# Kernel optimization log

Hardware: AMD Instinct MI355X
Metric: run time of the kernel (lower is better)

The kernel has to match this reference:

```python
import jax, jax.numpy as jnp
import numpy as np

EPS = 1e-5

def _act_quant(x):
    # per-token int8 absmax quantization with straight-through estimator
    scale = 127.0 / jnp.clip(jnp.max(jnp.abs(x), axis=-1, keepdims=True), EPS, None)
    q = jnp.clip(jnp.round(x * scale), -128.0, 127.0) / scale
    return x + jax.lax.stop_gradient(q - x)

def _weight_quant(w):
    # per-tensor ternary (1.58-bit) quantization with STE
    scale = 1.0 / jnp.clip(jnp.mean(jnp.abs(w)), EPS, None)
    q = jnp.clip(jnp.round(w * scale), -1.0, 1.0) / scale
    return w + jax.lax.stop_gradient(q - w)

def _bitlinear(x, w, b):
    y = jnp.einsum('bsd,od->bso', _act_quant(x), _weight_quant(w))
    return y + b

def setup_inputs() -> dict:
    key = jax.random.key(0)
    k1, k2, k3, k4, k5 = jax.random.split(key, 5)
    B, S, D, F = 8, 4096, 1024, 3072
    return {
        'x': jax.random.normal(k1, (B, S, D), dtype=jnp.float32),
        'up_w': jax.random.normal(k2, (F, D), dtype=jnp.float32) * 0.125,
        'up_b': jax.random.normal(k3, (F,), dtype=jnp.float32) * 0.01,
        'down_w': jax.random.normal(k4, (D, F), dtype=jnp.float32) * 0.125,
        'down_b': jax.random.normal(k5, (D,), dtype=jnp.float32) * 0.01,
    }

def reference(x, up_w, up_b, down_w, down_b):
    hidden = _bitlinear(x, up_w, up_b)          # [B,S,3072]
    hidden = jnp.square(jax.nn.relu(hidden))    # relu(h)^2
    return _bitlinear(hidden, down_w, down_b)   # [B,S,1024]
```

## Files before the change

kernel.cpp:

```cpp
#include <hip/hip_runtime.h>
#include <hip/hip_bf16.h>
#include <stdint.h>

#define EPS 1e-5f

typedef int v4i __attribute__((ext_vector_type(4)));
typedef int v16i __attribute__((ext_vector_type(16)));
typedef const __attribute__((address_space(1))) void g_void;
typedef __attribute__((address_space(3))) void l_void;

__device__ inline float block_max_nw(float v, int nw) {
    __shared__ float s[8];
#pragma unroll
    for (int o = 32; o; o >>= 1) v = fmaxf(v, __shfl_xor(v, o, 64));
    if ((threadIdx.x & 63) == 0) s[threadIdx.x >> 6] = v;
    __syncthreads();
    float m = s[0];
    for (int i = 1; i < nw; ++i) m = fmaxf(m, s[i]);
    return m;
}

__device__ inline float block_sum64x4(float v) {
    __shared__ float s[4];
#pragma unroll
    for (int o = 32; o; o >>= 1) v += __shfl_xor(v, o, 64);
    if ((threadIdx.x & 63) == 0) s[threadIdx.x >> 6] = v;
    __syncthreads();
    return s[0] + s[1] + s[2] + s[3];
}

__global__ __launch_bounds__(256) void abs_sum_part_k(const float4* __restrict__ w,
                                                      int n4, float* __restrict__ part) {
    float s = 0.0f;
    for (int i = blockIdx.x * 256 + threadIdx.x; i < n4; i += 1024 * 256) {
        float4 v = w[i];
        s += fabsf(v.x) + fabsf(v.y) + fabsf(v.z) + fabsf(v.w);
    }
    s = block_sum64x4(s);
    if (threadIdx.x == 0) part[blockIdx.x] = s;
}

__global__ __launch_bounds__(256) void abs_sum_final_k(const float* __restrict__ parts,
                                                       float* __restrict__ sums) {
    const float* p = parts + blockIdx.x * 1024;
    const int t = threadIdx.x;
    float s = p[t] + p[t + 256] + p[t + 512] + p[t + 768];
    s = block_sum64x4(s);
    if (t == 0) sums[blockIdx.x] = s;
}

__global__ __launch_bounds__(256) void wquant_k(const float4* __restrict__ w,
                                                char4* __restrict__ q,
                                                const float* __restrict__ sum) {
    const float mean = fmaxf(sum[0] * (1.0f / 3145728.0f), EPS);
    const float scale = 1.0f / mean;
    const int i = blockIdx.x * 256 + threadIdx.x;
    float4 v = w[i];
    char4 c;
    c.x = (signed char)(int)fmaxf(fminf(rintf(v.x * scale), 1.0f), -1.0f);
    c.y = (signed char)(int)fmaxf(fminf(rintf(v.y * scale), 1.0f), -1.0f);
    c.z = (signed char)(int)fmaxf(fminf(rintf(v.z * scale), 1.0f), -1.0f);
    c.w = (signed char)(int)fmaxf(fminf(rintf(v.w * scale), 1.0f), -1.0f);
    q[i] = c;
}

__global__ __launch_bounds__(256) void aquant_k(const float4* __restrict__ x,
                                                char4* __restrict__ q,
                                                float* __restrict__ deq) {
    const int row = blockIdx.x, t = threadIdx.x;
    const float4 v = x[(size_t)row * 256 + t];
    float m = fmaxf(fmaxf(fabsf(v.x), fabsf(v.y)), fmaxf(fabsf(v.z), fabsf(v.w)));
    m = block_max_nw(m, 4);
    const float mc = fmaxf(m, EPS);
    const float sc = 127.0f / mc;
    char4 c;
    c.x = (signed char)(int)fmaxf(fminf(rintf(v.x * sc), 127.0f), -128.0f);
    c.y = (signed char)(int)fmaxf(fminf(rintf(v.y * sc), 127.0f), -128.0f);
    c.z = (signed char)(int)fmaxf(fminf(rintf(v.z * sc), 127.0f), -128.0f);
    c.w = (signed char)(int)fmaxf(fminf(rintf(v.w * sc), 127.0f), -128.0f);
    q[(size_t)row * 256 + t] = c;
    if (t == 0) deq[row] = mc / 127.0f;
}

__global__ __launch_bounds__(384) void hquant_k(unsigned short* __restrict__ hid,
                                                float* __restrict__ deq) {
    const size_t row = blockIdx.x;
    const int t = threadIdx.x;
    unsigned short* rp = hid + row * 3072;
    const uint4 u = ((const uint4*)rp)[t];
    float v[8];
    {
        uint32_t uu[4] = {u.x, u.y, u.z, u.w};
#pragma unroll
        for (int i = 0; i < 4; ++i) {
            uint32_t lo = uu[i] << 16, hi = uu[i] & 0xFFFF0000u;
            v[2 * i]     = __uint_as_float(lo);
            v[2 * i + 1] = __uint_as_float(hi);
        }
    }
    float m = 0.0f;
#pragma unroll
    for (int i = 0; i < 8; ++i) m = fmaxf(m, fabsf(v[i]));
    m = block_max_nw(m, 6);
    const float mc = fmaxf(m, EPS);
    const float sc = 127.0f / mc;
    uint32_t p0 = 0, p1 = 0;
#pragma unroll
    for (int i = 0; i < 4; ++i) {
        int c = (int)fminf(rintf(v[i] * sc), 127.0f);
        p0 |= (uint32_t)(c & 255) << (8 * i);
    }
#pragma unroll
    for (int i = 0; i < 4; ++i) {
        int c = (int)fminf(rintf(v[4 + i] * sc), 127.0f);
        p1 |= (uint32_t)(c & 255) << (8 * i);
    }
    uint2 pk; pk.x = p0; pk.y = p1;
    ((uint2*)rp)[t] = pk;
    if (t == 0) deq[row] = mc / 127.0f;
}

template <bool RELU2, typename OutT>
__global__ __launch_bounds__(512, 2) void gemm_i8(
    const int8_t* __restrict__ A, int lda,
    const int8_t* __restrict__ B, int ldb,
    OutT* __restrict__ O, int ldo,
    const float* __restrict__ rowDeq,
    const float* __restrict__ sumPtr,
    const float* __restrict__ bias,
    int K, int nTiles) {
    __shared__ __align__(16) char As[4][16384];
    __shared__ __align__(16) char Bs[4][16384];
    const int t = threadIdx.x;
    const int lane = t & 63;
    const int w = t >> 6;
    const int wm = w >> 2;
    const int wn = w & 3;
    const int xcd = blockIdx.x & 7;
    const int sb = blockIdx.x >> 3;
    const int bm = xcd + 8 * (sb / nTiles);
    const int bn = sb % nTiles;
    const long m0 = (long)bm * 256;
    const long n0 = (long)bn * 256;

    v16i acc[4][2];
#pragma unroll
    for (int i = 0; i < 4; ++i)
#pragma unroll
        for (int j = 0; j < 2; ++j) acc[i][j] = (v16i)(0);

    const int r32 = lane & 31;
    const int h = lane >> 5;

    const int srow = lane >> 2;
    const int sc = ((lane & 3) ^ ((lane >> 3) & 3)) * 16;
    const int8_t* pa  = A + (m0 + 32 * w + srow) * (long)lda + sc;
    const int8_t* pb  = B + (n0 + 32 * w + srow) * (long)ldb + sc;
    const int8_t* pa1 = pa + 16 * (long)lda;
    const int8_t* pb1 = pb + 16 * (long)ldb;
    const int sdst = w * 2048;

    int cro[2];
#pragma unroll
    for (int ks = 0; ks < 2; ++ks) cro[ks] = ((2 * ks + h) ^ ((r32 >> 1) & 3)) * 16;
    const int arow = (wm * 128 + r32) * 64;
    const int brow = (wn * 64 + r32) * 64;

    const int NT = K >> 6;

    auto STAGE = [&](int tt) {
        const int buf = tt & 3;
        const long ko = (long)tt << 6;
        __builtin_amdgcn_global_load_lds((g_void*)(pa + ko),
                                         (l_void*)(As[buf] + sdst), 16, 0, 0);
        __builtin_amdgcn_global_load_lds((g_void*)(pa1 + ko),
                                         (l_void*)(As[buf] + sdst + 1024), 16, 0, 0);
        __builtin_amdgcn_global_load_lds((g_void*)(pb + ko),
                                         (l_void*)(Bs[buf] + sdst), 16, 0, 0);
        __builtin_amdgcn_global_load_lds((g_void*)(pb1 + ko),
                                         (l_void*)(Bs[buf] + sdst + 1024), 16, 0, 0);
    };

    STAGE(0);
    STAGE(1);
    STAGE(2);
    asm volatile("s_waitcnt vmcnt(8)" ::: "memory");
    __builtin_amdgcn_s_barrier();
    __builtin_amdgcn_sched_barrier(0);

    for (int tt = 0; tt < NT; ++tt) {
        const char* ab = As[tt & 3];
        const char* bb = Bs[tt & 3];
        if (tt + 3 < NT) STAGE(tt + 3);

        v4i af[4][2], bf[2][2];
#pragma unroll
        for (int mt = 0; mt < 4; ++mt)
#pragma unroll
            for (int ks = 0; ks < 2; ++ks)
                af[mt][ks] = *(const v4i*)(ab + arow + mt * 2048 + cro[ks]);
#pragma unroll
        for (int nt = 0; nt < 2; ++nt)
#pragma unroll
            for (int ks = 0; ks < 2; ++ks)
                bf[nt][ks] = *(const v4i*)(bb + brow + nt * 2048 + cro[ks]);

        __builtin_amdgcn_s_setprio(1);
#pragma unroll
        for (int ks = 0; ks < 2; ++ks)
#pragma unroll
            for (int mt = 0; mt < 4; ++mt)
#pragma unroll
                for (int nt = 0; nt < 2; ++nt)
                    acc[mt][nt] = __builtin_amdgcn_mfma_i32_32x32x32_i8(
                        af[mt][ks], bf[nt][ks], acc[mt][nt], 0, 0, 0);
        __builtin_amdgcn_s_setprio(0);

        if (tt + 3 < NT)      asm volatile("s_waitcnt vmcnt(8)" ::: "memory");
        else if (tt + 2 < NT) asm volatile("s_waitcnt vmcnt(4)" ::: "memory");
        else                  asm volatile("s_waitcnt vmcnt(0)" ::: "memory");
        __builtin_amdgcn_s_barrier();
        __builtin_amdgcn_sched_barrier(0);
    }

    const float wdeq = fmaxf(sumPtr[0] * (1.0f / 3145728.0f), EPS);
#pragma unroll
    for (int mt = 0; mt < 4; ++mt) {
#pragma unroll
        for (int g = 0; g < 4; ++g) {
#pragma unroll
            for (int rr = 0; rr < 4; ++rr) {
                const long row = m0 + wm * 128 + mt * 32 + g * 8 + h * 4 + rr;
                const float rs = rowDeq[row] * wdeq;
#pragma unroll
                for (int nt = 0; nt < 2; ++nt) {
                    const long col = n0 + wn * 64 + nt * 32 + r32;
                    float val = (float)acc[mt][nt][g * 4 + rr] * rs + bias[col];
                    if (RELU2) {
                        val = fmaxf(val, 0.0f);
                        val = val * val;
                    }
                    O[row * (long)ldo + col] = (OutT)val;
                }
            }
        }
    }
}

extern "C" void kernel_launch(void* const* d_in, const int* in_sizes, int n_in,
                              void* d_out, int out_size, void* d_ws, size_t ws_size,
                              hipStream_t stream) {
    const float* x      = (const float*)d_in[0];
    const float* up_w   = (const float*)d_in[1];
    const float* up_b   = (const float*)d_in[2];
    const float* down_w = (const float*)d_in[3];
    const float* down_b = (const float*)d_in[4];

    char* ws = (char*)d_ws;
    float*  sums   = (float*)ws;
    float*  parts  = (float*)(ws + 256);
    int8_t* qw_dn  = (int8_t*)(ws + 256 + 8192);
    float*  deqh   = (float*)(ws + 256 + 8192 + 3145728);
    __hip_bfloat16* hidden = (__hip_bfloat16*)(ws + 256 + 8192 + 3145728 + 131072);

    int8_t* qx    = (int8_t*)d_out;
    int8_t* qw_up = qx + 33554432;
    float*  deqx  = (float*)(qx + 33554432 + 3145728);

    abs_sum_part_k<<<1024, 256, 0, stream>>>((const float4*)up_w, 786432, parts);
    abs_sum_part_k<<<1024, 256, 0, stream>>>((const float4*)down_w, 786432, parts + 1024);
    abs_sum_final_k<<<2, 256, 0, stream>>>(parts, sums);

    wquant_k<<<3072, 256, 0, stream>>>((const float4*)up_w, (char4*)qw_up, &sums[0]);
    wquant_k<<<3072, 256, 0, stream>>>((const float4*)down_w, (char4*)qw_dn, &sums[1]);
    aquant_k<<<32768, 256, 0, stream>>>((const float4*)x, (char4*)qx, deqx);

    gemm_i8<true, __hip_bfloat16><<<1536, 512, 0, stream>>>(
        qx, 1024, qw_up, 1024, hidden, 3072, deqx, &sums[0], up_b, 1024, 12);
    hquant_k<<<32768, 384, 0, stream>>>((unsigned short*)hidden, deqh);
    gemm_i8<false, float><<<512, 512, 0, stream>>>(
        (const int8_t*)hidden, 6144, qw_dn, 3072, (float*)d_out, 1024,
        deqh, &sums[1], down_b, 3072, 4);
}
```

Baseline: 588.9 us.

## Restructure int8 GEMM mainloop into ping-pong double buffer with interleaved prefetch

The 4-stage 64-wide K pipeline is replaced by a 2-buffer scheme where each buffer holds two 64-K subtiles (128 K per iteration). Global-to-LDS prefetches for the next tile are spread across the MFMA sub-steps, with barriers after each quarter so memory issue and matrix math interleave. The LDS swizzle and the thread-to-row staging map also change. The aim is smoother overlap of loads and compute, at the cost of many more barriers per iteration and less prefetch depth.

```diff
diff --git a/kernel.cpp b/kernel.cpp
--- a/kernel.cpp
+++ b/kernel.cpp
@@ -129,8 +129,7 @@
     const float* __restrict__ sumPtr,
     const float* __restrict__ bias,
     int K, int nTiles) {
-    __shared__ __align__(16) char As[4][16384];
-    __shared__ __align__(16) char Bs[4][16384];
+    __shared__ __align__(16) char lds[2][65536];
     const int t = threadIdx.x;
     const int lane = t & 63;
     const int w = t >> 6;
@@ -152,75 +151,84 @@
     const int r32 = lane & 31;
     const int h = lane >> 5;
 
-    const int srow = lane >> 2;
-    const int sc = ((lane & 3) ^ ((lane >> 3) & 3)) * 16;
-    const int8_t* pa  = A + (m0 + 32 * w + srow) * (long)lda + sc;
-    const int8_t* pb  = B + (n0 + 32 * w + srow) * (long)ldb + sc;
-    const int8_t* pa1 = pa + 16 * (long)lda;
-    const int8_t* pb1 = pb + 16 * (long)ldb;
-    const int sdst = w * 2048;
+    const int srow = t >> 2;
+    const int scol = ((t & 3) ^ (srow & 3)) * 16;
+    const int8_t* srcA = A + (m0 + srow) * (long)lda + scol;
+    const int8_t* srcB = B + (n0 + srow) * (long)ldb + scol;
+    const long sA2 = 128 * (long)lda;
+    const long sB2 = 128 * (long)ldb;
 
     int cro[2];
 #pragma unroll
-    for (int ks = 0; ks < 2; ++ks) cro[ks] = ((2 * ks + h) ^ ((r32 >> 1) & 3)) * 16;
-    const int arow = (wm * 128 + r32) * 64;
-    const int brow = (wn * 64 + r32) * 64;
-
-    const int NT = K >> 6;
-
-    auto STAGE = [&](int tt) {
-        const int buf = tt & 3;
-        const long ko = (long)tt << 6;
-        __builtin_amdgcn_global_load_lds((g_void*)(pa + ko),
-                                         (l_void*)(As[buf] + sdst), 16, 0, 0);
-        __builtin_amdgcn_global_load_lds((g_void*)(pa1 + ko),
-                                         (l_void*)(As[buf] + sdst + 1024), 16, 0, 0);
-        __builtin_amdgcn_global_load_lds((g_void*)(pb + ko),
-                                         (l_void*)(Bs[buf] + sdst), 16, 0, 0);
-        __builtin_amdgcn_global_load_lds((g_void*)(pb1 + ko),
-                                         (l_void*)(Bs[buf] + sdst + 1024), 16, 0, 0);
-    };
-
-    STAGE(0);
-    STAGE(1);
-    STAGE(2);
-    asm volatile("s_waitcnt vmcnt(8)" ::: "memory");
+    for (int ks = 0; ks < 2; ++ks) cro[ks] = ((2 * ks + h) ^ (r32 & 3)) * 16;
+    const int abase = wm * 8192 + r32 * 64;
+    const int bbase = 16384 + wn * 4096 + r32 * 64;
+
+    const int NT = K >> 7;
+
+#pragma unroll
+    for (int p = 0; p < 8; ++p) {
+        const int kt = p >> 2, q = p & 3;
+        const long kg = (long)kt * 64;
+        l_void* d = (l_void*)(lds[0] + kt * 32768 + ((q & 2) ? 16384 : 0) +
+                              (q & 1) * 8192 + t * 16);
+        const g_void* s = (q & 2) ? (const g_void*)(srcB + (q & 1) * sB2 + kg)
+                                  : (const g_void*)(srcA + (q & 1) * sA2 + kg);
+        __builtin_amdgcn_global_load_lds(s, d, 16, 0, 0);
+    }
+    asm volatile("s_waitcnt vmcnt(4)" ::: "memory");
     __builtin_amdgcn_s_barrier();
     __builtin_amdgcn_sched_barrier(0);
 
     for (int tt = 0; tt < NT; ++tt) {
-        const char* ab = As[tt & 3];
-        const char* bb = Bs[tt & 3];
-        if (tt + 3 < NT) STAGE(tt + 3);
-
-        v4i af[4][2], bf[2][2];
-#pragma unroll
-        for (int mt = 0; mt < 4; ++mt)
-#pragma unroll
-            for (int ks = 0; ks < 2; ++ks)
-                af[mt][ks] = *(const v4i*)(ab + arow + mt * 2048 + cro[ks]);
-#pragma unroll
-        for (int nt = 0; nt < 2; ++nt)
-#pragma unroll
-            for (int ks = 0; ks < 2; ++ks)
-                bf[nt][ks] = *(const v4i*)(bb + brow + nt * 2048 + cro[ks]);
-
-        __builtin_amdgcn_s_setprio(1);
-#pragma unroll
-        for (int ks = 0; ks < 2; ++ks)
-#pragma unroll
-            for (int mt = 0; mt < 4; ++mt)
-#pragma unroll
-                for (int nt = 0; nt < 2; ++nt)
-                    acc[mt][nt] = __builtin_amdgcn_mfma_i32_32x32x32_i8(
-                        af[mt][ks], bf[nt][ks], acc[mt][nt], 0, 0, 0);
-        __builtin_amdgcn_s_setprio(0);
-
-        if (tt + 3 < NT)      asm volatile("s_waitcnt vmcnt(8)" ::: "memory");
-        else if (tt + 2 < NT) asm volatile("s_waitcnt vmcnt(4)" ::: "memory");
-        else                  asm volatile("s_waitcnt vmcnt(0)" ::: "memory");
-        __builtin_amdgcn_s_barrier();
-        __builtin_amdgcn_sched_barrier(0);
+        const char* base0 = lds[tt & 1];
+        char* nbuf = lds[(tt & 1) ^ 1];
+        const bool pf = (tt + 1 < NT);
+        const long kg1 = ((long)(tt + 1)) << 7;
+#pragma unroll
+        for (int kt = 0; kt < 2; ++kt) {
+            const char* base = base0 + kt * 32768;
+            v4i bf[2][2];
+#pragma unroll
+            for (int q = 0; q < 4; ++q) {
+                if (q == 0) {
+#pragma unroll
+                    for (int nt = 0; nt < 2; ++nt)
+#pragma unroll
+                        for (int ks = 0; ks < 2; ++ks)
+                            bf[nt][ks] = *(const v4i*)(base + bbase + nt * 2048 + cro[ks]);
+                }
+                v4i af[2];
+#pragma unroll
+                for (int ks = 0; ks < 2; ++ks)
+                    af[ks] = *(const v4i*)(base + abase + q * 2048 + cro[ks]);
+                if (pf) {
+                    const long kg = kg1 + kt * 64;
+                    l_void* d = (l_void*)(nbuf + kt * 32768 + ((q & 2) ? 16384 : 0) +
+                                          (q & 1) * 8192 + t * 16);
+                    const g_void* s = (q & 2)
+                        ? (const g_void*)(srcB + (q & 1) * sB2 + kg)
+                        : (const g_void*)(srcA + (q & 1) * sA2 + kg);
+                    __builtin_amdgcn_global_load_lds(s, d, 16, 0, 0);
+                }
+                __builtin_amdgcn_s_barrier();
+                __builtin_amdgcn_sched_barrier(0);
+                __builtin_amdgcn_s_setprio(1);
+#pragma unroll
+                for (int ks = 0; ks < 2; ++ks)
+#pragma unroll
+                    for (int nt = 0; nt < 2; ++nt)
+                        acc[q][nt] = __builtin_amdgcn_mfma_i32_32x32x32_i8(
+                            af[ks], bf[nt][ks], acc[q][nt], 0, 0, 0);
+                __builtin_amdgcn_s_setprio(0);
+                if (q == 3) {
+                    if (pf) asm volatile("s_waitcnt vmcnt(4)" ::: "memory");
+                    else    asm volatile("s_waitcnt vmcnt(0)" ::: "memory");
+                }
+                __builtin_amdgcn_s_barrier();
+                __builtin_amdgcn_sched_barrier(0);
+            }
+        }
     }
 
     const float wdeq = fmaxf(sumPtr[0] * (1.0f / 3145728.0f), EPS);
```

Measured after the change: 557.9 us. -5.3%, faster.
